# Performance work log

Hardware: AMD Instinct MI355X
Metric: run time of the kernel (lower is better)

## Reference

```python
import jax, jax.numpy as jnp
import numpy as np

K, T, F = 30000, 48, 4
EPS = 1e-5  # torch BatchNorm1d default eps


def _bn_params(key, c):
    k1, k2, k3, k4 = jax.random.split(key, 4)
    g = jax.random.uniform(k1, (c,), jnp.float32, 0.5, 1.5)
    b = jax.random.normal(k2, (c,), jnp.float32) * 0.1
    m = jax.random.normal(k3, (c,), jnp.float32) * 0.1
    v = jax.random.uniform(k4, (c,), jnp.float32, 0.5, 1.5)
    return g, b, m, v


def setup_inputs() -> dict:
    key = jax.random.key(0)
    ks = jax.random.split(key, 12)
    features = jax.random.normal(ks[0], (K, T, F), jnp.float32)
    # at least 1 valid point per non-empty voxel
    num_voxels = jnp.maximum(jax.random.randint(ks[1], (K,), 0, T), 1).astype(jnp.int32)
    coors = jax.random.randint(ks[2], (K, 3), 0, 100).astype(jnp.int32)
    # VFE1: in=8 (4 + 3 rel + 1 dist), units = 32//2 = 16
    w1 = jax.random.normal(ks[3], (8, 16), jnp.float32) / np.sqrt(8)
    b1 = jax.random.normal(ks[4], (16,), jnp.float32) * 0.01
    g1, be1, m1, v1 = _bn_params(ks[5], 16)
    # VFE2: in=32, units = 128//2 = 64
    w2 = jax.random.normal(ks[6], (32, 64), jnp.float32) / np.sqrt(32)
    b2 = jax.random.normal(ks[7], (64,), jnp.float32) * 0.01
    g2, be2, m2, v2 = _bn_params(ks[8], 64)
    # final linear 128 -> 128
    w3 = jax.random.normal(ks[9], (128, 128), jnp.float32) / np.sqrt(128)
    b3 = jax.random.normal(ks[10], (128,), jnp.float32) * 0.01
    g3, be3, m3, v3 = _bn_params(ks[11], 128)
    return dict(features=features, num_voxels=num_voxels, coors=coors,
                w1=w1, b1=b1, g1=g1, be1=be1, m1=m1, v1=v1,
                w2=w2, b2=b2, g2=g2, be2=be2, m2=m2, v2=v2,
                w3=w3, b3=b3, g3=g3, be3=be3, m3=m3, v3=v3)


def _bn(x, g, b, m, v):
    # eval-mode BatchNorm over last (channel) axis
    return (x - m) * (g / jnp.sqrt(v + EPS)) + b


def _vfe(x, W, b, g, be, m, v):
    # x: [K, T, Cin] -> [K, T, 2*units]
    h = jax.nn.relu(_bn(jnp.einsum('ktc,cu->ktu', x, W) + b, g, be, m, v))
    agg = jnp.max(h, axis=1, keepdims=True)  # [K, 1, U]
    return jnp.concatenate([h, jnp.broadcast_to(agg, h.shape)], axis=2)


def reference(features, num_voxels, coors,
              w1, b1, g1, be1, m1, v1,
              w2, b2, g2, be2, m2, v2,
              w3, b3, g3, be3, m3, v3):
    xyz = features[:, :, :3]
    nv = num_voxels.astype(features.dtype)[:, None, None]
    points_mean = jnp.sum(xyz, axis=1, keepdims=True) / nv
    rel = xyz - points_mean
    dist = jnp.linalg.norm(xyz, axis=2, keepdims=True)
    x = jnp.concatenate([features, rel, dist], axis=-1)  # [K, T, 8]
    mask = (jnp.arange(T)[None, :] < num_voxels[:, None]).astype(features.dtype)[:, :, None]
    x = x * mask
    x = _vfe(x, w1, b1, g1, be1, m1, v1) * mask   # [K, T, 32]
    x = _vfe(x, w2, b2, g2, be2, m2, v2) * mask   # [K, T, 128]
    x = jax.nn.relu(_bn(jnp.einsum('ktc,cu->ktu', x, w3) + b3, g3, be3, m3, v3)) * mask
    return jnp.max(x, axis=1)  # [K, 128]
```

## Files before the change

kernel.cpp:

```cpp
#include <hip/hip_runtime.h>

constexpr float EPS = 1e-5f;

typedef __attribute__((ext_vector_type(8))) short bf16x8;
typedef __attribute__((ext_vector_type(4))) float f32x4;

#define W2P_OFF 32768
#define W1P_OFF 40960
#define B1_OFF  41984
#define B2_OFF  42048
#define B3_OFF  42304

__device__ __forceinline__ ushort f2bf(float x) {
    union { float f; unsigned u; } a; a.f = x;
    unsigned r = a.u + 0x7fffu + ((a.u >> 16) & 1u);
    return (ushort)(r >> 16);
}

__device__ __forceinline__ unsigned cvtpk(float lo, float hi) {
    unsigned r;
    asm("v_cvt_pk_bf16_f32 %0, %1, %2" : "=v"(r) : "v"(lo), "v"(hi));
    return r;
}

__global__ void vfe_prep(
    const float* __restrict__ w1, const float* __restrict__ b1,
    const float* __restrict__ g1, const float* __restrict__ be1,
    const float* __restrict__ m1, const float* __restrict__ v1,
    const float* __restrict__ w2, const float* __restrict__ b2,
    const float* __restrict__ g2, const float* __restrict__ be2,
    const float* __restrict__ m2, const float* __restrict__ v2,
    const float* __restrict__ w3, const float* __restrict__ b3,
    const float* __restrict__ g3, const float* __restrict__ be3,
    const float* __restrict__ m3, const float* __restrict__ v3,
    void* __restrict__ ws)
{
    ushort* w3p = (ushort*)ws;
    ushort* w2p = (ushort*)((char*)ws + W2P_OFF);
    ushort* w1p = (ushort*)((char*)ws + W1P_OFF);
    float*  bb1 = (float*)((char*)ws + B1_OFF);
    float*  bb2 = (float*)((char*)ws + B2_OFF);
    float*  bb3 = (float*)((char*)ws + B3_OFF);

    const int i = blockIdx.x * 256 + threadIdx.x;
    if (i < 16384) {
        const int e = i & 7, l = (i >> 3) & 63, rest = i >> 9;
        const int ks = rest & 3, nt = rest >> 2, g = l >> 4;
        const int k = ks * 32 + g * 8 + e;
        const int n = nt * 16 + (l & 15);
        const float s = g3[n] * rsqrtf(v3[n] + EPS);
        w3p[i] = f2bf(w3[k * 128 + n] * s);
    } else if (i < 20480) {
        const int j = i - 16384;
        const int e = j & 7, l = (j >> 3) & 63, rest = j >> 9;
        const int nt = rest & 3, sel = rest >> 2;
        const int klog = (l >> 4) * 8 + e;
        const int n = nt * 16 + (l & 15);
        const float s = g2[n] * rsqrtf(v2[n] + EPS);
        w2p[j] = (klog < 16) ? f2bf(w2[(sel * 16 + klog) * 64 + n] * s) : (ushort)0;
    } else if (i < 20992) {
        const int j = i - 20480;
        const int e = j & 7, l = j >> 3;
        const int klog = (l >> 4) * 8 + e;
        const int u = l & 15;
        const float s = g1[u] * rsqrtf(v1[u] + EPS);
        w1p[j] = (klog < 8) ? f2bf(w1[klog * 16 + u] * s) : (ushort)0;
    } else if (i < 21200) {
        const int j = i - 20992;
        if (j < 16) {
            const int u = j;
            bb1[u] = (b1[u] - m1[u]) * (g1[u] * rsqrtf(v1[u] + EPS)) + be1[u];
        } else if (j < 80) {
            const int u = j - 16;
            bb2[u] = (b2[u] - m2[u]) * (g2[u] * rsqrtf(v2[u] + EPS)) + be2[u];
        } else {
            const int u = j - 80;
            bb3[u] = (b3[u] - m3[u]) * (g3[u] * rsqrtf(v3[u] + EPS)) + be3[u];
        }
    }
}

__global__ __launch_bounds__(256, 4) void vfe_fused(
    const float* __restrict__ feat,
    const int* __restrict__ nvox,
    const void* __restrict__ ws,
    float* __restrict__ out,
    int K)
{
    __shared__ __align__(16) ushort sX0bf[96][8];
    __shared__ __align__(16) ushort sAfrag[6 * 16 * 24];
    __shared__ __align__(16) ushort sBfrag[6 * 2 * 64 * 8];
    __shared__ float  sP[6][17];
    __shared__ __align__(16) ushort sAgg1bf[2][16];
    __shared__ __align__(16) ushort sAgg2bf[2][64];

    const ushort* w3p = (const ushort*)ws;
    const ushort* w2p = (const ushort*)((const char*)ws + W2P_OFF);
    const ushort* w1p = (const ushort*)((const char*)ws + W1P_OFF);
    const float*  bb1 = (const float*)((const char*)ws + B1_OFF);
    const float*  bb2 = (const float*)((const char*)ws + B2_OFF);
    const float*  bb3 = (const float*)((const char*)ws + B3_OFF);

    const int tid  = threadIdx.x;
    const int lane = tid & 63;
    const int w    = tid >> 6;
    const int g    = lane >> 4;
    const int m15  = lane & 15;
    const int kA   = blockIdx.x * 2;
    const int kB   = kA + 1;
    const bool hasB = (kB < K);
    int nvA = nvox[kA];
    nvA = __builtin_amdgcn_readfirstlane(nvA);
    int nvB = hasB ? nvox[kB] : 1;
    nvB = __builtin_amdgcn_readfirstlane(nvB);
    const int limA  = (nvA + 15) >> 4;
    const int limB  = (nvB + 15) >> 4;
    const int fullA = nvA >> 4;
    const int fullB = nvB >> 4;

    union U8 { bf16x8 v; unsigned u[4]; };

    const bf16x8 b1f   = *(const bf16x8*)(w1p + (size_t)lane * 8);
    const bf16x8 w2lof = *(const bf16x8*)(w2p + (size_t)((0 * 4 + w) * 64 + lane) * 8);
    const bf16x8 w2hif = *(const bf16x8*)(w2p + (size_t)((1 * 4 + w) * 64 + lane) * 8);
    bf16x8 b3f[2][4];
    #pragma unroll
    for (int nt = 0; nt < 2; ++nt)
        #pragma unroll
        for (int ks = 0; ks < 4; ++ks)
            b3f[nt][ks] = *(const bf16x8*)(w3p + (size_t)(((w * 2 + nt) * 4 + ks) * 64 + lane) * 8);

    if (w < 2) {
        const int vox = w;
        const int nv  = vox ? nvB : nvA;
        const int kk  = vox ? kB : kA;
        float4 f = make_float4(0.f, 0.f, 0.f, 0.f);
        if (lane < 48 && (vox == 0 || hasB))
            f = *reinterpret_cast<const float4*>(feat + ((size_t)kk * 48 + lane) * 4);
        float sx = f.x, sy = f.y, sz = f.z;
        #pragma unroll
        for (int d = 1; d < 64; d <<= 1) {
            sx += __shfl_xor(sx, d);
            sy += __shfl_xor(sy, d);
            sz += __shfl_xor(sz, d);
        }
        const float inv = 1.f / (float)nv;
        if (lane < 48) {
            const float msk = (lane < nv) ? 1.f : 0.f;
            const float dd = sqrtf(f.x * f.x + f.y * f.y + f.z * f.z);
            U8 a;
            a.u[0] = cvtpk(f.x * msk, f.y * msk);
            a.u[1] = cvtpk(f.z * msk, f.w * msk);
            a.u[2] = cvtpk((f.x - sx * inv) * msk, (f.y - sy * inv) * msk);
            a.u[3] = cvtpk((f.z - sz * inv) * msk, dd * msk);
            *reinterpret_cast<bf16x8*>(&sX0bf[vox * 48 + lane][0]) = a.v;
        }
    }
    __syncthreads();

    {
        const float bia = bb1[m15];
        #pragma unroll
        for (int slot = 0; slot < 2; ++slot) {
            if (slot == 0 || w < 2) {
                const int tt  = (slot == 0) ? w : (w + 4);
                const int vox = (tt >= 3) ? 1 : 0;
                const int mtl = tt - vox * 3;
                const int limV = vox ? limB : limA;
                if (mtl < limV) {
                    const bf16x8 af = *(const bf16x8*)&sX0bf[tt * 16 + m15][0];
                    f32x4 ci = {bia, bia, bia, bia};
                    f32x4 acc = __builtin_amdgcn_mfma_f32_16x16x32_bf16(af, b1f, ci, 0, 0, 0);
                    float pmax = 0.f;
                    #pragma unroll
                    for (int r = 0; r < 4; ++r) {
                        const float h = fmaxf(acc[r], 0.f);
                        pmax = fmaxf(pmax, h);
                        sAfrag[(tt * 16 + g * 4 + r) * 24 + m15] = f2bf(h);
                    }
                    pmax = fmaxf(pmax, __shfl_xor(pmax, 16));
                    pmax = fmaxf(pmax, __shfl_xor(pmax, 32));
                    if (lane < 16) sP[tt][m15] = pmax;
                }
            }
        }
    }
    __syncthreads();
    if (tid < 32) {
        const int u = tid & 15, vox = tid >> 4;
        const int limV = vox ? limB : limA;
        float mx = fmaxf(bb1[u], 0.f);
        #pragma unroll
        for (int tb = 0; tb < 3; ++tb)
            if (tb < limV) mx = fmaxf(mx, sP[vox * 3 + tb][u]);
        sAgg1bf[vox][u] = f2bf(mx);
    }
    __syncthreads();

    const int col2 = w * 16 + m15;
    const float bb2c = bb2[col2];
    f32x4 z2acc;
    {
        const bf16x8 az2 = *(const bf16x8*)&sAgg1bf[m15 & 1][(g & 1) * 8];
        f32x4 ci = {bb2c, bb2c, bb2c, bb2c};
        z2acc = __builtin_amdgcn_mfma_f32_16x16x32_bf16(az2, w2hif, ci, 0, 0, 0);
    }
    const float iA2 = z2acc[0];
    const float iB2 = z2acc[1];

    f32x4 acc2[6];
    #pragma unroll
    for (int mt = 0; mt < 6; ++mt) {
        const int vox = (mt >= 3);
        const int limV = vox ? limB : limA;
        if ((mt - vox * 3) < limV) {
            const bf16x8 af = *(const bf16x8*)&sAfrag[(mt * 16 + m15) * 24 + (g & 1) * 8];
            const float ci = vox ? iB2 : iA2;
            f32x4 c = {ci, ci, ci, ci};
            acc2[mt] = __builtin_amdgcn_mfma_f32_16x16x32_bf16(af, w2lof, c, 0, 0, 0);
        }
    }
    {
        const int ks = col2 >> 5, gp = (col2 >> 3) & 3, e = col2 & 7;
        float mxA = fmaxf(bb2c, 0.f);
        float mxB = fmaxf(bb2c, 0.f);
        #pragma unroll
        for (int mt = 0; mt < 6; ++mt) {
            const int vox = (mt >= 3);
            const int nv    = vox ? nvB : nvA;
            const int limV  = vox ? limB : limA;
            const int fullV = vox ? fullB : fullA;
            const int mtl = mt - vox * 3;
            if (mtl < limV) {
                float h[4];
                #pragma unroll
                for (int r = 0; r < 4; ++r) {
                    h[r] = fmaxf(acc2[mt][r], 0.f);
                    sBfrag[((mt * 2 + ks) * 64 + gp * 16 + (g * 4 + r)) * 8 + e] = f2bf(h[r]);
                }
                if (mtl < fullV) {
                    float t01 = fmaxf(h[0], h[1]), t23 = fmaxf(h[2], h[3]);
                    if (vox) mxB = fmaxf(mxB, fmaxf(t01, t23));
                    else     mxA = fmaxf(mxA, fmaxf(t01, t23));
                } else {
                    #pragma unroll
                    for (int r = 0; r < 4; ++r) {
                        if (mtl * 16 + g * 4 + r < nv) {
                            if (vox) mxB = fmaxf(mxB, h[r]);
                            else     mxA = fmaxf(mxA, h[r]);
                        }
                    }
                }
            }
        }
        mxA = fmaxf(mxA, __shfl_xor(mxA, 16));
        mxA = fmaxf(mxA, __shfl_xor(mxA, 32));
        mxB = fmaxf(mxB, __shfl_xor(mxB, 16));
        mxB = fmaxf(mxB, __shfl_xor(mxB, 32));
        if (g == 0) {
            sAgg2bf[0][col2] = f2bf(mxA);
            sAgg2bf[1][col2] = f2bf(mxB);
        }
    }
    __syncthreads();

    float iA3[2], iB3[2];
    #pragma unroll
    for (int nt = 0; nt < 2; ++nt) {
        const float bb3c = bb3[(w * 2 + nt) * 16 + m15];
        f32x4 z = {bb3c, bb3c, bb3c, bb3c};
        #pragma unroll
        for (int ks2 = 0; ks2 < 2; ++ks2) {
            const bf16x8 af = *(const bf16x8*)&sAgg2bf[m15 & 1][ks2 * 32 + g * 8];
            z = __builtin_amdgcn_mfma_f32_16x16x32_bf16(af, b3f[nt][2 + ks2], z, 0, 0, 0);
        }
        iA3[nt] = z[0];
        iB3[nt] = z[1];
    }

    #pragma unroll
    for (int pass = 0; pass < 2; ++pass) {
        f32x4 acc3[6];
        #pragma unroll
        for (int mt = 0; mt < 6; ++mt) {
            const int vox = (mt >= 3);
            const int limV = vox ? limB : limA;
            if ((mt - vox * 3) < limV) {
                const bf16x8 af0 = *(const bf16x8*)&sBfrag[((mt * 2 + 0) * 64 + lane) * 8];
                const bf16x8 af1 = *(const bf16x8*)&sBfrag[((mt * 2 + 1) * 64 + lane) * 8];
                const float ci = vox ? iB3[pass] : iA3[pass];
                f32x4 c = {ci, ci, ci, ci};
                acc3[mt] = __builtin_amdgcn_mfma_f32_16x16x32_bf16(af0, b3f[pass][0], c, 0, 0, 0);
                acc3[mt] = __builtin_amdgcn_mfma_f32_16x16x32_bf16(af1, b3f[pass][1], acc3[mt], 0, 0, 0);
            }
        }
        const int col = (w * 2 + pass) * 16 + m15;
        float mxA = 0.f, mxB = 0.f;
        #pragma unroll
        for (int mt = 0; mt < 3; ++mt) {
            if (mt < fullA) {
                float t01 = fmaxf(acc3[mt][0], acc3[mt][1]);
                float t23 = fmaxf(acc3[mt][2], acc3[mt][3]);
                mxA = fmaxf(mxA, fmaxf(t01, t23));
            } else if (mt < limA) {
                #pragma unroll
                for (int r = 0; r < 4; ++r)
                    if (mt * 16 + g * 4 + r < nvA) mxA = fmaxf(mxA, acc3[mt][r]);
            }
            if (mt < fullB) {
                float t01 = fmaxf(acc3[mt + 3][0], acc3[mt + 3][1]);
                float t23 = fmaxf(acc3[mt + 3][2], acc3[mt + 3][3]);
                mxB = fmaxf(mxB, fmaxf(t01, t23));
            } else if (mt < limB) {
                #pragma unroll
                for (int r = 0; r < 4; ++r)
                    if (mt * 16 + g * 4 + r < nvB) mxB = fmaxf(mxB, acc3[mt + 3][r]);
            }
        }
        mxA = fmaxf(mxA, __shfl_xor(mxA, 16));
        mxA = fmaxf(mxA, __shfl_xor(mxA, 32));
        mxB = fmaxf(mxB, __shfl_xor(mxB, 16));
        mxB = fmaxf(mxB, __shfl_xor(mxB, 32));
        if (g == 0) out[(size_t)kA * 128 + col] = mxA;
        if (g == 1 && hasB) out[(size_t)kB * 128 + col] = mxB;
    }
}

extern "C" void kernel_launch(void* const* d_in, const int* in_sizes, int n_in,
                              void* d_out, int out_size, void* d_ws, size_t ws_size,
                              hipStream_t stream) {
    const float* feat = (const float*)d_in[0];
    const int*   nvx  = (const int*)d_in[1];
    const float* w1 = (const float*)d_in[3];
    const float* b1 = (const float*)d_in[4];
    const float* g1 = (const float*)d_in[5];
    const float* be1= (const float*)d_in[6];
    const float* m1 = (const float*)d_in[7];
    const float* v1 = (const float*)d_in[8];
    const float* w2 = (const float*)d_in[9];
    const float* b2 = (const float*)d_in[10];
    const float* g2 = (const float*)d_in[11];
    const float* be2= (const float*)d_in[12];
    const float* m2 = (const float*)d_in[13];
    const float* v2 = (const float*)d_in[14];
    const float* w3 = (const float*)d_in[15];
    const float* b3 = (const float*)d_in[16];
    const float* g3 = (const float*)d_in[17];
    const float* be3= (const float*)d_in[18];
    const float* m3 = (const float*)d_in[19];
    const float* v3 = (const float*)d_in[20];
    float* out = (float*)d_out;

    const int K = in_sizes[1];

    vfe_prep<<<84, 256, 0, stream>>>(w1,b1,g1,be1,m1,v1, w2,b2,g2,be2,m2,v2,
                                     w3,b3,g3,be3,m3,v3, d_ws);
    vfe_fused<<<(K + 1) / 2, 256, 0, stream>>>(feat, nvx, d_ws, out, K);
}
```

Measured before the change: 75.41 us.

## Process four voxels per block instead of two in fused VFE kernel

Each 256-thread block now handles four voxels, one per wave, for feature preprocessing and the first layer. This amortizes the per-block weight-fragment loads and barriers over twice as many voxels and halves the grid size. The first-layer max is now reduced inside each wave, which removes one shared-memory partial buffer and one __syncthreads. The cost is larger shared-memory use and more register pressure from the wider accumulator loops, which may lower occupancy.

```diff
diff --git a/kernel.cpp b/kernel.cpp
--- a/kernel.cpp
+++ b/kernel.cpp
@@ -80,6 +80,10 @@
     }
 }
 
+#define NV(v)   ((v)==0?nv0:(v)==1?nv1:(v)==2?nv2:nv3)
+#define LIM(v)  ((v)==0?lim0:(v)==1?lim1:(v)==2?lim2:lim3)
+#define FULL(v) ((v)==0?full0:(v)==1?full1:(v)==2?full2:full3)
+
 __global__ __launch_bounds__(256, 4) void vfe_fused(
     const float* __restrict__ feat,
     const int* __restrict__ nvox,
@@ -87,12 +91,11 @@
     float* __restrict__ out,
     int K)
 {
-    __shared__ __align__(16) ushort sX0bf[96][8];
-    __shared__ __align__(16) ushort sAfrag[6 * 16 * 24];
-    __shared__ __align__(16) ushort sBfrag[6 * 2 * 64 * 8];
-    __shared__ float  sP[6][17];
-    __shared__ __align__(16) ushort sAgg1bf[2][16];
-    __shared__ __align__(16) ushort sAgg2bf[2][64];
+    __shared__ __align__(16) ushort sX0bf[192][8];
+    __shared__ __align__(16) ushort sAfrag[12 * 16 * 24];
+    __shared__ __align__(16) ushort sBfrag[12 * 2 * 64 * 8];
+    __shared__ __align__(16) ushort sAgg1bf[4][16];
+    __shared__ __align__(16) ushort sAgg2bf[4][64];
 
     const ushort* w3p = (const ushort*)ws;
     const ushort* w2p = (const ushort*)((const char*)ws + W2P_OFF);
@@ -106,17 +109,15 @@
     const int w    = tid >> 6;
     const int g    = lane >> 4;
     const int m15  = lane & 15;
-    const int kA   = blockIdx.x * 2;
-    const int kB   = kA + 1;
-    const bool hasB = (kB < K);
-    int nvA = nvox[kA];
-    nvA = __builtin_amdgcn_readfirstlane(nvA);
-    int nvB = hasB ? nvox[kB] : 1;
-    nvB = __builtin_amdgcn_readfirstlane(nvB);
-    const int limA  = (nvA + 15) >> 4;
-    const int limB  = (nvB + 15) >> 4;
-    const int fullA = nvA >> 4;
-    const int fullB = nvB >> 4;
+    const int kA   = blockIdx.x * 4;
+
+    int kk0 = kA, kk1 = min(kA+1, K-1), kk2 = min(kA+2, K-1), kk3 = min(kA+3, K-1);
+    int nv0 = __builtin_amdgcn_readfirstlane(nvox[kk0]);
+    int nv1 = __builtin_amdgcn_readfirstlane(nvox[kk1]);
+    int nv2 = __builtin_amdgcn_readfirstlane(nvox[kk2]);
+    int nv3 = __builtin_amdgcn_readfirstlane(nvox[kk3]);
+    const int lim0=(nv0+15)>>4, lim1=(nv1+15)>>4, lim2=(nv2+15)>>4, lim3=(nv3+15)>>4;
+    const int full0=nv0>>4, full1=nv1>>4, full2=nv2>>4, full3=nv3>>4;
 
     union U8 { bf16x8 v; unsigned u[4]; };
 
@@ -130,13 +131,12 @@
         for (int ks = 0; ks < 4; ++ks)
             b3f[nt][ks] = *(const bf16x8*)(w3p + (size_t)(((w * 2 + nt) * 4 + ks) * 64 + lane) * 8);
 
-    if (w < 2) {
-        const int vox = w;
-        const int nv  = vox ? nvB : nvA;
-        const int kk  = vox ? kB : kA;
+    {
+        const int kkw = (w==0)?kk0:(w==1)?kk1:(w==2)?kk2:kk3;
+        const int nvw = (w==0)?nv0:(w==1)?nv1:(w==2)?nv2:nv3;
         float4 f = make_float4(0.f, 0.f, 0.f, 0.f);
-        if (lane < 48 && (vox == 0 || hasB))
-            f = *reinterpret_cast<const float4*>(feat + ((size_t)kk * 48 + lane) * 4);
+        if (lane < 48)
+            f = *reinterpret_cast<const float4*>(feat + ((size_t)kkw * 48 + lane) * 4);
         float sx = f.x, sy = f.y, sz = f.z;
         #pragma unroll
         for (int d = 1; d < 64; d <<= 1) {
@@ -144,56 +144,41 @@
             sy += __shfl_xor(sy, d);
             sz += __shfl_xor(sz, d);
         }
-        const float inv = 1.f / (float)nv;
+        const float inv = 1.f / (float)nvw;
         if (lane < 48) {
-            const float msk = (lane < nv) ? 1.f : 0.f;
+            const float msk = (lane < nvw) ? 1.f : 0.f;
             const float dd = sqrtf(f.x * f.x + f.y * f.y + f.z * f.z);
             U8 a;
             a.u[0] = cvtpk(f.x * msk, f.y * msk);
             a.u[1] = cvtpk(f.z * msk, f.w * msk);
             a.u[2] = cvtpk((f.x - sx * inv) * msk, (f.y - sy * inv) * msk);
             a.u[3] = cvtpk((f.z - sz * inv) * msk, dd * msk);
-            *reinterpret_cast<bf16x8*>(&sX0bf[vox * 48 + lane][0]) = a.v;
+            *reinterpret_cast<bf16x8*>(&sX0bf[w * 48 + lane][0]) = a.v;
         }
     }
     __syncthreads();
 
     {
-        const float bia = bb1[m15];
-        #pragma unroll
-        for (int slot = 0; slot < 2; ++slot) {
-            if (slot == 0 || w < 2) {
-                const int tt  = (slot == 0) ? w : (w + 4);
-                const int vox = (tt >= 3) ? 1 : 0;
-                const int mtl = tt - vox * 3;
-                const int limV = vox ? limB : limA;
-                if (mtl < limV) {
-                    const bf16x8 af = *(const bf16x8*)&sX0bf[tt * 16 + m15][0];
-                    f32x4 ci = {bia, bia, bia, bia};
-                    f32x4 acc = __builtin_amdgcn_mfma_f32_16x16x32_bf16(af, b1f, ci, 0, 0, 0);
-                    float pmax = 0.f;
-                    #pragma unroll
-                    for (int r = 0; r < 4; ++r) {
-                        const float h = fmaxf(acc[r], 0.f);
-                        pmax = fmaxf(pmax, h);
-                        sAfrag[(tt * 16 + g * 4 + r) * 24 + m15] = f2bf(h);
-                    }
-                    pmax = fmaxf(pmax, __shfl_xor(pmax, 16));
-                    pmax = fmaxf(pmax, __shfl_xor(pmax, 32));
-                    if (lane < 16) sP[tt][m15] = pmax;
-                }
-            }
-        }
-    }
-    __syncthreads();
-    if (tid < 32) {
-        const int u = tid & 15, vox = tid >> 4;
-        const int limV = vox ? limB : limA;
-        float mx = fmaxf(bb1[u], 0.f);
-        #pragma unroll
-        for (int tb = 0; tb < 3; ++tb)
-            if (tb < limV) mx = fmaxf(mx, sP[vox * 3 + tb][u]);
-        sAgg1bf[vox][u] = f2bf(mx);
+        const float bb1u = bb1[m15];
+        const int limw = (w==0)?lim0:(w==1)?lim1:(w==2)?lim2:lim3;
+        float pmax = fmaxf(bb1u, 0.f);
+        #pragma unroll
+        for (int s = 0; s < 3; ++s) {
+            if (s < limw) {
+                const bf16x8 af = *(const bf16x8*)&sX0bf[w * 48 + s * 16 + m15][0];
+                f32x4 ci = {bb1u, bb1u, bb1u, bb1u};
+                f32x4 acc = __builtin_amdgcn_mfma_f32_16x16x32_bf16(af, b1f, ci, 0, 0, 0);
+                #pragma unroll
+                for (int r = 0; r < 4; ++r) {
+                    const float h = fmaxf(acc[r], 0.f);
+                    pmax = fmaxf(pmax, h);
+                    sAfrag[((w * 3 + s) * 16 + g * 4 + r) * 24 + m15] = f2bf(h);
+                }
+            }
+        }
+        pmax = fmaxf(pmax, __shfl_xor(pmax, 16));
+        pmax = fmaxf(pmax, __shfl_xor(pmax, 32));
+        if (g == 0) sAgg1bf[w][m15] = f2bf(pmax);
     }
     __syncthreads();
 
@@ -201,128 +186,129 @@
     const float bb2c = bb2[col2];
     f32x4 z2acc;
     {
-        const bf16x8 az2 = *(const bf16x8*)&sAgg1bf[m15 & 1][(g & 1) * 8];
+        const bf16x8 az2 = *(const bf16x8*)&sAgg1bf[m15 & 3][(g & 1) * 8];
         f32x4 ci = {bb2c, bb2c, bb2c, bb2c};
         z2acc = __builtin_amdgcn_mfma_f32_16x16x32_bf16(az2, w2hif, ci, 0, 0, 0);
     }
-    const float iA2 = z2acc[0];
-    const float iB2 = z2acc[1];
-
-    f32x4 acc2[6];
-    #pragma unroll
-    for (int mt = 0; mt < 6; ++mt) {
-        const int vox = (mt >= 3);
-        const int limV = vox ? limB : limA;
-        if ((mt - vox * 3) < limV) {
-            const bf16x8 af = *(const bf16x8*)&sAfrag[(mt * 16 + m15) * 24 + (g & 1) * 8];
-            const float ci = vox ? iB2 : iA2;
-            f32x4 c = {ci, ci, ci, ci};
-            acc2[mt] = __builtin_amdgcn_mfma_f32_16x16x32_bf16(af, w2lof, c, 0, 0, 0);
-        }
-    }
+
     {
         const int ks = col2 >> 5, gp = (col2 >> 3) & 3, e = col2 & 7;
-        float mxA = fmaxf(bb2c, 0.f);
-        float mxB = fmaxf(bb2c, 0.f);
-        #pragma unroll
-        for (int mt = 0; mt < 6; ++mt) {
-            const int vox = (mt >= 3);
-            const int nv    = vox ? nvB : nvA;
-            const int limV  = vox ? limB : limA;
-            const int fullV = vox ? fullB : fullA;
-            const int mtl = mt - vox * 3;
-            if (mtl < limV) {
-                float h[4];
-                #pragma unroll
-                for (int r = 0; r < 4; ++r) {
-                    h[r] = fmaxf(acc2[mt][r], 0.f);
-                    sBfrag[((mt * 2 + ks) * 64 + gp * 16 + (g * 4 + r)) * 8 + e] = f2bf(h[r]);
-                }
-                if (mtl < fullV) {
-                    float t01 = fmaxf(h[0], h[1]), t23 = fmaxf(h[2], h[3]);
-                    if (vox) mxB = fmaxf(mxB, fmaxf(t01, t23));
-                    else     mxA = fmaxf(mxA, fmaxf(t01, t23));
-                } else {
+        #pragma unroll
+        for (int vg = 0; vg < 2; ++vg) {
+            f32x4 acc2[6];
+            #pragma unroll
+            for (int j = 0; j < 6; ++j) {
+                const int tt = vg * 6 + j;
+                const int vox = vg * 2 + j / 3;
+                const int mtl = j % 3;
+                if (mtl < LIM(vox)) {
+                    const bf16x8 af = *(const bf16x8*)&sAfrag[(tt * 16 + m15) * 24 + (g & 1) * 8];
+                    const float ci = z2acc[vox];
+                    f32x4 c = {ci, ci, ci, ci};
+                    acc2[j] = __builtin_amdgcn_mfma_f32_16x16x32_bf16(af, w2lof, c, 0, 0, 0);
+                }
+            }
+            float mxP = fmaxf(bb2c, 0.f);
+            float mxQ = fmaxf(bb2c, 0.f);
+            #pragma unroll
+            for (int j = 0; j < 6; ++j) {
+                const int tt = vg * 6 + j;
+                const int vox = vg * 2 + j / 3;
+                const int mtl = j % 3;
+                if (mtl < LIM(vox)) {
+                    float h[4];
                     #pragma unroll
                     for (int r = 0; r < 4; ++r) {
-                        if (mtl * 16 + g * 4 + r < nv) {
-                            if (vox) mxB = fmaxf(mxB, h[r]);
-                            else     mxA = fmaxf(mxA, h[r]);
+                        h[r] = fmaxf(acc2[j][r], 0.f);
+                        sBfrag[((tt * 2 + ks) * 64 + gp * 16 + (g * 4 + r)) * 8 + e] = f2bf(h[r]);
+                    }
+                    if (mtl < FULL(vox)) {
+                        const float t01 = fmaxf(h[0], h[1]), t23 = fmaxf(h[2], h[3]);
+                        if (j < 3) mxP = fmaxf(mxP, fmaxf(t01, t23));
+                        else       mxQ = fmaxf(mxQ, fmaxf(t01, t23));
+                    } else {
+                        #pragma unroll
+                        for (int r = 0; r < 4; ++r) {
+                            if (mtl * 16 + g * 4 + r < NV(vox)) {
+                                if (j < 3) mxP = fmaxf(mxP, h[r]);
+                                else       mxQ = fmaxf(mxQ, h[r]);
+                            }
                         }
                     }
                 }
             }
-        }
-        mxA = fmaxf(mxA, __shfl_xor(mxA, 16));
-        mxA = fmaxf(mxA, __shfl_xor(mxA, 32));
-        mxB = fmaxf(mxB, __shfl_xor(mxB, 16));
-        mxB = fmaxf(mxB, __shfl_xor(mxB, 32));
-        if (g == 0) {
-            sAgg2bf[0][col2] = f2bf(mxA);
-            sAgg2bf[1][col2] = f2bf(mxB);
+            mxP = fmaxf(mxP, __shfl_xor(mxP, 16));
+            mxP = fmaxf(mxP, __shfl_xor(mxP, 32));
+            mxQ = fmaxf(mxQ, __shfl_xor(mxQ, 16));
+            mxQ = fmaxf(mxQ, __shfl_xor(mxQ, 32));
+            if (g == 0) {
+                sAgg2bf[vg * 2 + 0][col2] = f2bf(mxP);
+                sAgg2bf[vg * 2 + 1][col2] = f2bf(mxQ);
+            }
         }
     }
     __syncthreads();
 
-    float iA3[2], iB3[2];
+    f32x4 i3[2];
     #pragma unroll
     for (int nt = 0; nt < 2; ++nt) {
         const float bb3c = bb3[(w * 2 + nt) * 16 + m15];
         f32x4 z = {bb3c, bb3c, bb3c, bb3c};
         #pragma unroll
         for (int ks2 = 0; ks2 < 2; ++ks2) {
-            const bf16x8 af = *(const bf16x8*)&sAgg2bf[m15 & 1][ks2 * 32 + g * 8];
+            const bf16x8 af = *(const bf16x8*)&sAgg2bf[m15 & 3][ks2 * 32 + g * 8];
             z = __builtin_amdgcn_mfma_f32_16x16x32_bf16(af, b3f[nt][2 + ks2], z, 0, 0, 0);
         }
-        iA3[nt] = z[0];
-        iB3[nt] = z[1];
+        i3[nt] = z;
     }
 
     #pragma unroll
     for (int pass = 0; pass < 2; ++pass) {
-        f32x4 acc3[6];
-        #pragma unroll
-        for (int mt = 0; mt < 6; ++mt) {
-            const int vox = (mt >= 3);
-            const int limV = vox ? limB : limA;
-            if ((mt - vox * 3) < limV) {
-                const bf16x8 af0 = *(const bf16x8*)&sBfrag[((mt * 2 + 0) * 64 + lane) * 8];
-                const bf16x8 af1 = *(const bf16x8*)&sBfrag[((mt * 2 + 1) * 64 + lane) * 8];
-                const float ci = vox ? iB3[pass] : iA3[pass];
-                f32x4 c = {ci, ci, ci, ci};
-                acc3[mt] = __builtin_amdgcn_mfma_f32_16x16x32_bf16(af0, b3f[pass][0], c, 0, 0, 0);
-                acc3[mt] = __builtin_amdgcn_mfma_f32_16x16x32_bf16(af1, b3f[pass][1], acc3[mt], 0, 0, 0);
-            }
-        }
         const int col = (w * 2 + pass) * 16 + m15;
-        float mxA = 0.f, mxB = 0.f;
-        #pragma unroll
-        for (int mt = 0; mt < 3; ++mt) {
-            if (mt < fullA) {
-                float t01 = fmaxf(acc3[mt][0], acc3[mt][1]);
-                float t23 = fmaxf(acc3[mt][2], acc3[mt][3]);
-                mxA = fmaxf(mxA, fmaxf(t01, t23));
-            } else if (mt < limA) {
-                #pragma unroll
-                for (int r = 0; r < 4; ++r)
-                    if (mt * 16 + g * 4 + r < nvA) mxA = fmaxf(mxA, acc3[mt][r]);
-            }
-            if (mt < fullB) {
-                float t01 = fmaxf(acc3[mt + 3][0], acc3[mt + 3][1]);
-                float t23 = fmaxf(acc3[mt + 3][2], acc3[mt + 3][3]);
-                mxB = fmaxf(mxB, fmaxf(t01, t23));
-            } else if (mt < limB) {
-                #pragma unroll
-                for (int r = 0; r < 4; ++r)
-                    if (mt * 16 + g * 4 + r < nvB) mxB = fmaxf(mxB, acc3[mt + 3][r]);
-            }
-        }
-        mxA = fmaxf(mxA, __shfl_xor(mxA, 16));
-        mxA = fmaxf(mxA, __shfl_xor(mxA, 32));
-        mxB = fmaxf(mxB, __shfl_xor(mxB, 16));
-        mxB = fmaxf(mxB, __shfl_xor(mxB, 32));
-        if (g == 0) out[(size_t)kA * 128 + col] = mxA;
-        if (g == 1 && hasB) out[(size_t)kB * 128 + col] = mxB;
+        #pragma unroll
+        for (int vg = 0; vg < 2; ++vg) {
+            f32x4 acc3[6];
+            #pragma unroll
+            for (int j = 0; j < 6; ++j) {
+                const int tt = vg * 6 + j;
+                const int vox = vg * 2 + j / 3;
+                const int mtl = j % 3;
+                if (mtl < LIM(vox)) {
+                    const bf16x8 af0 = *(const bf16x8*)&sBfrag[((tt * 2 + 0) * 64 + lane) * 8];
+                    const bf16x8 af1 = *(const bf16x8*)&sBfrag[((tt * 2 + 1) * 64 + lane) * 8];
+                    const float ci = i3[pass][vox];
+                    f32x4 c = {ci, ci, ci, ci};
+                    acc3[j] = __builtin_amdgcn_mfma_f32_16x16x32_bf16(af0, b3f[pass][0], c, 0, 0, 0);
+                    acc3[j] = __builtin_amdgcn_mfma_f32_16x16x32_bf16(af1, b3f[pass][1], acc3[j], 0, 0, 0);
+                }
+            }
+            float mxP = 0.f, mxQ = 0.f;
+            #pragma unroll
+            for (int j = 0; j < 6; ++j) {
+                const int vox = vg * 2 + j / 3;
+                const int mtl = j % 3;
+                if (mtl < FULL(vox)) {
+                    const float t01 = fmaxf(acc3[j][0], acc3[j][1]);
+                    const float t23 = fmaxf(acc3[j][2], acc3[j][3]);
+                    if (j < 3) mxP = fmaxf(mxP, fmaxf(t01, t23));
+                    else       mxQ = fmaxf(mxQ, fmaxf(t01, t23));
+                } else if (mtl < LIM(vox)) {
+                    #pragma unroll
+                    for (int r = 0; r < 4; ++r) {
+                        if (mtl * 16 + g * 4 + r < NV(vox)) {
+                            if (j < 3) mxP = fmaxf(mxP, acc3[j][r]);
+                            else       mxQ = fmaxf(mxQ, acc3[j][r]);
+                        }
+                    }
+                }
+            }
+            mxP = fmaxf(mxP, __shfl_xor(mxP, 16));
+            mxP = fmaxf(mxP, __shfl_xor(mxP, 32));
+            mxQ = fmaxf(mxQ, __shfl_xor(mxQ, 16));
+            mxQ = fmaxf(mxQ, __shfl_xor(mxQ, 32));
+            if (g == (vg * 2 + 0) && (kA + vg * 2 + 0) < K) out[(size_t)(kA + vg * 2 + 0) * 128 + col] = mxP;
+            if (g == (vg * 2 + 1) && (kA + vg * 2 + 1) < K) out[(size_t)(kA + vg * 2 + 1) * 128 + col] = mxQ;
+        }
     }
 }
 
@@ -355,5 +341,5 @@
 
     vfe_prep<<<84, 256, 0, stream>>>(w1,b1,g1,be1,m1,v1, w2,b2,g2,be2,m2,v2,
                                      w3,b3,g3,be3,m3,v3, d_ws);
-    vfe_fused<<<(K + 1) / 2, 256, 0, stream>>>(feat, nvx, d_ws, out, K);
-}
+    vfe_fused<<<(K + 3) / 4, 256, 0, stream>>>(feat, nvx, d_ws, out, K);
+}
```

Result: no change. 73.97 us (-1.9%).
